# Kernel tuning notes

Measured on AMD Instinct MI355X. Metric: run time of the kernel, lower is better.

## Reference

```python
import jax, jax.numpy as jnp
import numpy as np

L, B, S, D, H, FF = 6, 32, 512, 512, 8, 2048
DK = D // H
EPS = 1e-5
GELU_C = 0.7978845608028654  # sqrt(2/pi)
INV_SQRT_DK = 1.0 / float(np.sqrt(DK))


def gelu(x):
    return 0.5 * x * (1.0 + jnp.tanh(GELU_C * (x + 0.044715 * x ** 3)))


def layernorm(x, gamma, beta):
    m = jnp.mean(x, axis=-1, keepdims=True)
    v = jnp.mean(jnp.square(x - m), axis=-1, keepdims=True)
    return gamma * (x - m) / jnp.sqrt(v + EPS) + beta


def attention(x, WQ, WK, WV, WO):
    # NOTE: the original splits columns as (d_key, n_heads) on input,
    # and merges as (n_heads * d_key) on output -- replicated faithfully.
    q = (x @ WQ).reshape(B, S, DK, H).transpose(0, 3, 1, 2)  # (B,H,S,DK)
    k = (x @ WK).reshape(B, S, DK, H).transpose(0, 3, 2, 1)  # (B,H,DK,S)
    v = (x @ WV).reshape(B, S, DK, H).transpose(0, 3, 1, 2)  # (B,H,S,DK)
    score = jax.nn.softmax(jnp.matmul(q, k) * INV_SQRT_DK, axis=-1)  # (B,H,S,S)
    o = jnp.matmul(score, v).transpose(0, 2, 1, 3).reshape(B, S, H * DK)
    return o @ WO


def setup_inputs() -> dict:
    key = jax.random.key(0)
    ks = jax.random.split(key, 8)
    sc = 0.02
    return {
        "x": jax.random.normal(ks[0], (B, S, D), jnp.float32),
        "WQ": jax.random.normal(ks[1], (L, D, D), jnp.float32) * sc,
        "WK": jax.random.normal(ks[2], (L, D, D), jnp.float32) * sc,
        "WV": jax.random.normal(ks[3], (L, D, D), jnp.float32) * sc,
        "WO": jax.random.normal(ks[4], (L, D, D), jnp.float32) * sc,
        "K1": jax.random.normal(ks[5], (L, D, FF), jnp.float32) * sc,
        "B1": jnp.zeros((L, FF), jnp.float32),
        "K2": jax.random.normal(ks[6], (L, FF, D), jnp.float32) * sc,
        "B2": jnp.zeros((L, D), jnp.float32),
        "G1": jnp.ones((L, D), jnp.float32),
        "BE1": jnp.zeros((L, D), jnp.float32),
        "G2": jnp.ones((L, D), jnp.float32),
        "BE2": jnp.zeros((L, D), jnp.float32),
    }


def reference(x, WQ, WK, WV, WO, K1, B1, K2, B2, G1, BE1, G2, BE2):
    def step(h, p):
        wq, wk, wv, wo, k1, b1, k2, b2, g1, be1, g2, be2 = p
        h = layernorm(h + attention(h, wq, wk, wv, wo), g1, be1)
        f = gelu(h @ k1 + b1) @ k2 + b2
        h = layernorm(h + f, g2, be2)
        return h, None

    out, _ = jax.lax.scan(step, x, (WQ, WK, WV, WO, K1, B1, K2, B2, G1, BE1, G2, BE2))
    return out
```

## Files before the change

kernel.cpp:

```cpp
#include <hip/hip_runtime.h>
#include <hip/hip_bf16.h>
#include <stdint.h>

#define LB 6
#define BB 32
#define SS 512
#define DD 512
#define HH 8
#define FF_ 2048
#define MM (BB*SS)

typedef unsigned short u16;
typedef __attribute__((ext_vector_type(8))) short bf16x8;
typedef __attribute__((ext_vector_type(4))) float f32x4;

#define MFMA16(a,b,c) __builtin_amdgcn_mfma_f32_16x16x32_bf16((a),(b),(c),0,0,0)
#define GLD16(g, l) __builtin_amdgcn_global_load_lds( \
    (const __attribute__((address_space(1))) unsigned int*)(g), \
    (__attribute__((address_space(3))) unsigned int*)(l), 16, 0, 0)
#define BAR() asm volatile("s_barrier" ::: "memory")
#define VMW(n) asm volatile("s_waitcnt vmcnt(" #n ")" ::: "memory")

__device__ __forceinline__ u16 f2b(float f){
  unsigned int u = __float_as_uint(f);
  u = u + 0x7FFFu + ((u >> 16) & 1u);
  return (u16)(u >> 16);
}

__device__ __forceinline__ float gelu_f(float x){
  float u2 = 1.5957691216057308f * (x + 0.044715f * x * x * x);
  return x / (1.0f + __expf(-u2));
}

__global__ __launch_bounds__(256) void k_prep(const float* __restrict__ x,
                                              float* __restrict__ h,
                                              u16* __restrict__ hb){
  int i = blockIdx.x * 256 + threadIdx.x;
  float4 v = ((const float4*)x)[i];
  ((float4*)h)[i] = v;
  uint2 p;
  p.x = (unsigned)f2b(v.x) | ((unsigned)f2b(v.y) << 16);
  p.y = (unsigned)f2b(v.z) | ((unsigned)f2b(v.w) << 16);
  ((uint2*)hb)[i] = p;
}

__global__ __launch_bounds__(256) void k_wt(const float* __restrict__ in,
                                            u16* __restrict__ out, int K, int N){
  size_t ms = (size_t)K * N;
  in  += ms * blockIdx.z;
  out += ms * blockIdx.z;
  int n0 = blockIdx.x * 64, k0 = blockIdx.y * 64;
  __shared__ float tile[64][65];
  int t = threadIdx.x;
  int c = t & 63, rb = t >> 6;
  #pragma unroll
  for (int p = 0; p < 16; p++){
    int k = p * 4 + rb;
    tile[k][c] = in[(size_t)(k0 + k) * N + (n0 + c)];
  }
  __syncthreads();
  #pragma unroll
  for (int p = 0; p < 16; p++){
    int n = p * 4 + rb;
    out[(size_t)(n0 + n) * K + (k0 + c)] = f2b(tile[c][n]);
  }
}

template<int BN, int EPI, bool PERM>
__global__ __launch_bounds__(512, 1) void k_gemm8(
    const u16* __restrict__ A,
    const u16* __restrict__ Bq, const u16* __restrict__ Bk, const u16* __restrict__ Bv,
    const float* __restrict__ bias, float* __restrict__ outF, u16* __restrict__ outH,
    int N, int K)
{
  constexpr int WM = (BN==256) ? 2 : 4;
  constexpr int MR = 16/WM;
  constexpr int MQ = MR/4;
  constexpr int BHALF = (BN==256) ? 8192 : 4096;
  constexpr int BBUF  = 2*BHALF;
  constexpr int BL    = (BN==256) ? 2 : 1;
  constexpr int HC    = (BN==256) ? 128 : 64;
  __shared__ u16 sM[32768 + 2*BBUF];

  const int t = threadIdx.x;
  const int lane = t & 63, w = t >> 6, lr = lane & 15, lh = lane >> 4;
  const int wm = (BN==256) ? (w>>2) : (w>>1);
  const int wn = (BN==256) ? (w&3)  : (w&1);
  const int bm = blockIdx.x * 256, bn = blockIdx.y * BN;
  const int NTT = K >> 6, NIT = NTT >> 1;
  const int tz = PERM ? (bn >> 9) : 0;

  const int skA = (((t>>6)&1)<<5) + (((t>>4)&3)<<3);
  const int srA = ((t>>7)<<4) + (t&15);
  const u16* gA0 = A + (size_t)(bm +       srA) * K + skA;
  const u16* gA1 = A + (size_t)(bm + 128 + srA) * K + skA;
  const u16* gBp[2][2];
  {
    const u16* Bsel = PERM ? (tz==0 ? Bq : tz==1 ? Bk : Bv) : Bq;
    #pragma unroll
    for (int h = 0; h < 2; h++){
      #pragma unroll
      for (int s = 0; s < BL; s++){
        int n = (PERM ? (bn & 511) : bn) + h*HC + srA + s*64;
        int srow = PERM ? (((n & 63) << 3) | (n >> 6)) : n;
        gBp[h][s] = Bsel + (size_t)srow * K + skA;
      }
    }
  }

  auto stageA = [&](int kt, int h){
    u16* dst = sM + (kt&1)*16384 + h*8192 + t*8;
    const u16* src = (h ? gA1 : gA0) + kt*64;
    GLD16(src, dst);
    GLD16(src + (size_t)64*K, dst + 4096);
  };
  auto stageB = [&](int kt, int h){
    u16* dst = sM + 32768 + (kt&1)*BBUF + h*BHALF + t*8;
    GLD16(gBp[h][0] + kt*64, dst);
    if constexpr (BL == 2) GLD16(gBp[h][1] + kt*64, dst + 4096);
  };

  const int ha    = (BN==256) ? wm : (wm>>1);
  const int mbase = (BN==256) ? 0  : ((wm&1)*4);
  const int hbi   = (BN==256) ? (wn>>1) : wn;
  const int nfb   = (BN==256) ? ((wn&1)*4) : 0;
  const int rdAbase = ha*8192 + lane*8;
  const int rdBbase = 32768 + hbi*BHALF + nfb*1024 + lane*8;

  f32x4 acc[MR][4];
  #pragma unroll
  for (int i = 0; i < MR; i++)
    #pragma unroll
    for (int j = 0; j < 4; j++) acc[i][j] = (f32x4){0.f,0.f,0.f,0.f};
  bf16x8 bfr[4][2];

#define RD_A(d, q, af) { _Pragma("unroll") for (int i=0;i<MQ;i++){ _Pragma("unroll") for (int ks=0;ks<2;ks++) \
    af[i][ks] = *(const bf16x8*)&sM[(d)*16384 + rdAbase + ((mbase + (q)*MQ + i)*2 + ks)*512]; } }
#define RD_B(d) { _Pragma("unroll") for (int j=0;j<4;j++){ _Pragma("unroll") for (int ks=0;ks<2;ks++) \
    bfr[j][ks] = *(const bf16x8*)&sM[(d)*BBUF + rdBbase + ((j)*2 + (ks))*512]; } }
#define FMA_Q(q, af) { __builtin_amdgcn_s_setprio(1); \
  _Pragma("unroll") for (int i=0;i<MQ;i++){ _Pragma("unroll") for (int j=0;j<4;j++){ _Pragma("unroll") for (int ks=0;ks<2;ks++) \
    acc[(q)*MQ+i][j] = MFMA16(af[i][ks], bfr[j][ks], acc[(q)*MQ+i][j]); } } \
  __builtin_amdgcn_s_setprio(0); }

  stageA(0,0); stageA(0,1); stageB(0,0); stageB(0,1); stageB(1,0); stageB(1,1);
  if constexpr (BL == 2) { VMW(4); } else { VMW(2); }
  BAR();

  for (int it = 0; it < NIT; ++it){
    const int t0 = it*2;
    const bool lastit = (it == NIT-1);
    bf16x8 af[MQ][2];
    RD_A(0,0,af); RD_B(0); stageA(t0+1, 0);            BAR(); FMA_Q(0, af); BAR();
    RD_A(0,1,af);          stageA(t0+1, 1);            BAR(); FMA_Q(1, af); BAR();
    RD_A(0,2,af); if (t0+2 < NTT) stageB(t0+2, 0);     BAR(); FMA_Q(2, af); BAR();
    RD_A(0,3,af); if (t0+2 < NTT) stageB(t0+2, 1);     BAR(); FMA_Q(3, af);
    if (lastit) { VMW(0); } else { if constexpr (BL == 2) { VMW(4); } else { VMW(2); } }
    BAR();
    RD_A(1,0,af); RD_B(1); if (t0+2 < NTT) stageA(t0+2, 0); BAR(); FMA_Q(0, af); BAR();
    RD_A(1,1,af);          if (t0+2 < NTT) stageA(t0+2, 1); BAR(); FMA_Q(1, af); BAR();
    RD_A(1,2,af); if (t0+3 < NTT) stageB(t0+3, 0);     BAR(); FMA_Q(2, af); BAR();
    RD_A(1,3,af); if (t0+3 < NTT) stageB(t0+3, 1);     BAR(); FMA_Q(3, af);
    if (!lastit) { if constexpr (BL == 2) { VMW(4); } else { VMW(2); } }
    BAR();
  }
#undef RD_A
#undef RD_B
#undef FMA_Q

  #pragma unroll
  for (int mf = 0; mf < MR; mf++){
    const int row = bm + wm*(256/WM) + mf*16 + lh*4;
    #pragma unroll
    for (int j = 0; j < 4; j++){
      const int col = (PERM ? (bn & 511) : bn) + wn*64 + j*16 + lr;
      float bv = (EPI >= 2) ? bias[col] : 0.f;
      #pragma unroll
      for (int r = 0; r < 4; r++){
        float v = acc[mf][j][r];
        size_t o = (size_t)(row + r) * N + col;
        if (PERM) o += (size_t)tz * ((size_t)MM * DD);
        if (EPI == 0) outH[o] = f2b(v);
        else if (EPI == 1) outF[o] = v;
        else if (EPI == 2) outH[o] = f2b(gelu_f(v + bv));
        else outF[o] = v + bv;
      }
    }
  }
}

__global__ __launch_bounds__(256) void k_attn(const u16* __restrict__ Q, const u16* __restrict__ Kp,
                                              const u16* __restrict__ V, u16* __restrict__ O){
  const int qt = blockIdx.x, hh = blockIdx.y, b = blockIdx.z;
  __shared__ u16 Qs[64*64];
  __shared__ u16 Ks[64*64];
  __shared__ u16 Vt[64*64];
  __shared__ u16 Ps[64*64];
  const int t = threadIdx.x, w = t >> 6, lane = t & 63, lr = lane & 15, lh = lane >> 4;
  const size_t base = ((size_t)b * SS) * DD + (size_t)hh * 64;

  const int srow = t >> 3;
  const int gcol = (((t & 7) ^ (srow & 7)) << 3);
  {
    const u16* g = Q + base + (size_t)(qt*64 + srow) * DD + gcol;
    GLD16(g,                   Qs + w*512);
    GLD16(g + (size_t)32*DD,   Qs + 2048 + w*512);
  }

  float mreg[4], lreg[4];
  f32x4 ofr[4];
  #pragma unroll
  for (int r = 0; r < 4; r++){ mreg[r] = -1e30f; lreg[r] = 0.f; }
  #pragma unroll
  for (int j = 0; j < 4; j++) ofr[j] = (f32x4){0.f,0.f,0.f,0.f};

  const int qswz = (lr & 7) << 3;

  for (int kt = 0; kt < 8; kt++){
    {
      const u16* g = Kp + base + (size_t)(kt*64 + srow) * DD + gcol;
      GLD16(g,                 Ks + w*512);
      GLD16(g + (size_t)32*DD, Ks + 2048 + w*512);
    }
    {
      const int dk0 = (t & 7) * 8, kv = (t >> 3) * 2;
      const u16* g = V + base + (size_t)(kt*64 + kv) * DD + dk0;
      uint4 r0 = *(const uint4*)g;
      uint4 r1 = *(const uint4*)(g + DD);
      const u16* e0 = (const u16*)&r0;
      const u16* e1 = (const u16*)&r1;
      #pragma unroll
      for (int i = 0; i < 8; i++){
        int dk = dk0 + i;
        int sw = ((((dk >> 3) ^ dk) & 7) << 3);
        *(unsigned int*)&Vt[dk*64 + (kv ^ sw)] =
            (unsigned int)e0[i] | ((unsigned int)e1[i] << 16);
      }
    }
    __syncthreads();

    bf16x8 a0 = *(const bf16x8*)&Qs[(w*16+lr)*64 + ((lh*8) ^ qswz)];
    bf16x8 a1 = *(const bf16x8*)&Qs[(w*16+lr)*64 + ((32 + lh*8) ^ qswz)];
    f32x4 sc[4];
    #pragma unroll
    for (int j = 0; j < 4; j++){
      bf16x8 b0 = *(const bf16x8*)&Ks[(j*16+lr)*64 + ((lh*8) ^ qswz)];
      bf16x8 b1 = *(const bf16x8*)&Ks[(j*16+lr)*64 + ((32 + lh*8) ^ qswz)];
      f32x4 z = (f32x4){0.f,0.f,0.f,0.f};
      z = MFMA16(a0, b0, z);
      z = MFMA16(a1, b1, z);
      sc[j] = z;
    }

    float pr[4][4];
    float esc[4];
    #pragma unroll
    for (int r = 0; r < 4; r++){
      float mx = fmaxf(fmaxf(sc[0][r], sc[1][r]), fmaxf(sc[2][r], sc[3][r]));
      mx = fmaxf(mx, __shfl_xor(mx, 1));
      mx = fmaxf(mx, __shfl_xor(mx, 2));
      mx = fmaxf(mx, __shfl_xor(mx, 4));
      mx = fmaxf(mx, __shfl_xor(mx, 8));
      mx *= 0.125f;
      float m2 = fmaxf(mreg[r], mx);
      float scl = __expf(mreg[r] - m2);
      mreg[r] = m2;
      float s = 0.f;
      #pragma unroll
      for (int j = 0; j < 4; j++){
        float p = __expf(sc[j][r]*0.125f - m2);
        pr[j][r] = p;
        s += p;
      }
      s += __shfl_xor(s, 1);
      s += __shfl_xor(s, 2);
      s += __shfl_xor(s, 4);
      s += __shfl_xor(s, 8);
      lreg[r] = lreg[r]*scl + s;
      esc[r] = scl;
    }

    #pragma unroll
    for (int j = 0; j < 4; j++)
      #pragma unroll
      for (int r = 0; r < 4; r++){
        int prow = w*16 + lh*4 + r;
        int pcol = j*16 + lr;
        Ps[prow*64 + (pcol ^ (((lh*4 + r) & 7) << 3))] = f2b(pr[j][r]);
      }

    #pragma unroll
    for (int j = 0; j < 4; j++)
      #pragma unroll
      for (int r = 0; r < 4; r++) ofr[j][r] *= esc[r];

    bf16x8 pa0 = *(const bf16x8*)&Ps[(w*16+lr)*64 + ((lh*8) ^ qswz)];
    bf16x8 pa1 = *(const bf16x8*)&Ps[(w*16+lr)*64 + ((32 + lh*8) ^ qswz)];
    #pragma unroll
    for (int j = 0; j < 4; j++){
      int dkr = j*16 + lr;
      int sw = ((((dkr >> 3) ^ dkr) & 7) << 3);
      bf16x8 v0 = *(const bf16x8*)&Vt[dkr*64 + ((lh*8) ^ sw)];
      bf16x8 v1 = *(const bf16x8*)&Vt[dkr*64 + ((32 + lh*8) ^ sw)];
      ofr[j] = MFMA16(pa0, v0, ofr[j]);
      ofr[j] = MFMA16(pa1, v1, ofr[j]);
    }
    __syncthreads();
  }

  #pragma unroll
  for (int j = 0; j < 4; j++)
    #pragma unroll
    for (int r = 0; r < 4; r++){
      float v = ofr[j][r] / lreg[r];
      O[base + (size_t)(qt*64 + w*16 + lh*4 + r) * DD + j*16 + lr] = f2b(v);
    }
}

__global__ __launch_bounds__(256) void k_ln(const float* __restrict__ hin, const float* __restrict__ add,
    const float* __restrict__ g, const float* __restrict__ be,
    float* __restrict__ hout, u16* __restrict__ hb){
  const int w = threadIdx.x >> 6, lane = threadIdx.x & 63;
  const size_t row = (size_t)blockIdx.x * 4 + w;
  const size_t base = row * DD + lane * 8;
  float4 xa = *(const float4*)&hin[base];
  float4 xb = *(const float4*)&hin[base + 4];
  float4 aa = *(const float4*)&add[base];
  float4 ab = *(const float4*)&add[base + 4];
  float v[8] = { xa.x+aa.x, xa.y+aa.y, xa.z+aa.z, xa.w+aa.w,
                 xb.x+ab.x, xb.y+ab.y, xb.z+ab.z, xb.w+ab.w };
  float s = 0.f, q = 0.f;
  #pragma unroll
  for (int e = 0; e < 8; e++){ s += v[e]; q += v[e]*v[e]; }
  #pragma unroll
  for (int m = 32; m >= 1; m >>= 1){ s += __shfl_xor(s, m); q += __shfl_xor(q, m); }
  float mean = s * (1.f/512.f);
  float var  = q * (1.f/512.f) - mean*mean;
  float rstd = rsqrtf(var + 1e-5f);
  float4 g0 = *(const float4*)&g[lane*8],  g1 = *(const float4*)&g[lane*8+4];
  float4 b0 = *(const float4*)&be[lane*8], b1 = *(const float4*)&be[lane*8+4];
  float gv[8] = {g0.x,g0.y,g0.z,g0.w,g1.x,g1.y,g1.z,g1.w};
  float bv[8] = {b0.x,b0.y,b0.z,b0.w,b1.x,b1.y,b1.z,b1.w};
  float o[8];
  #pragma unroll
  for (int e = 0; e < 8; e++) o[e] = gv[e] * ((v[e]-mean)*rstd) + bv[e];
  *(float4*)&hout[base]     = make_float4(o[0],o[1],o[2],o[3]);
  *(float4*)&hout[base + 4] = make_float4(o[4],o[5],o[6],o[7]);
  uint4 pk;
  pk.x = (unsigned)f2b(o[0]) | ((unsigned)f2b(o[1])<<16);
  pk.y = (unsigned)f2b(o[2]) | ((unsigned)f2b(o[3])<<16);
  pk.z = (unsigned)f2b(o[4]) | ((unsigned)f2b(o[5])<<16);
  pk.w = (unsigned)f2b(o[6]) | ((unsigned)f2b(o[7])<<16);
  *(uint4*)&hb[base] = pk;
}

extern "C" void kernel_launch(void* const* d_in, const int* in_sizes, int n_in,
                              void* d_out, int out_size, void* d_ws, size_t ws_size,
                              hipStream_t stream){
  const float* x   = (const float*)d_in[0];
  const float* WQ  = (const float*)d_in[1];
  const float* WK  = (const float*)d_in[2];
  const float* WV  = (const float*)d_in[3];
  const float* WO  = (const float*)d_in[4];
  const float* K1  = (const float*)d_in[5];
  const float* B1  = (const float*)d_in[6];
  const float* K2  = (const float*)d_in[7];
  const float* B2  = (const float*)d_in[8];
  const float* G1  = (const float*)d_in[9];
  const float* BE1 = (const float*)d_in[10];
  const float* G2  = (const float*)d_in[11];
  const float* BE2 = (const float*)d_in[12];
  float* hF = (float*)d_out;

  char* wp = (char*)d_ws;
  size_t off = 0;
  auto a16 = [&](size_t elems)->u16*{ u16* p = (u16*)(wp + off); off += elems*sizeof(u16); return p; };
  u16* WQt = a16((size_t)LB*DD*DD);
  u16* WKt = a16((size_t)LB*DD*DD);
  u16* WVt = a16((size_t)LB*DD*DD);
  u16* WOt = a16((size_t)LB*DD*DD);
  u16* K1t = a16((size_t)LB*DD*FF_);
  u16* K2t = a16((size_t)LB*DD*FF_);
  u16* hbf = a16((size_t)MM*DD);
  u16* qbf = a16((size_t)MM*DD);
  u16* kbf = a16((size_t)MM*DD);
  u16* vbf = a16((size_t)MM*DD);
  u16* abf = a16((size_t)MM*DD);
  u16* ff1 = qbf;
  float* tmpF = (float*)(wp + off); off += (size_t)MM*DD*sizeof(float);
  (void)ws_size; (void)in_sizes; (void)n_in; (void)out_size;

  k_prep<<<MM*DD/4/256, 256, 0, stream>>>(x, hF, hbf);
  k_wt<<<dim3(8,8,LB),        256, 0, stream>>>(WQ, WQt, DD, DD);
  k_wt<<<dim3(8,8,LB),        256, 0, stream>>>(WK, WKt, DD, DD);
  k_wt<<<dim3(8,8,LB),        256, 0, stream>>>(WV, WVt, DD, DD);
  k_wt<<<dim3(8,8,LB),        256, 0, stream>>>(WO, WOt, DD, DD);
  k_wt<<<dim3(FF_/64,8,LB),   256, 0, stream>>>(K1, K1t, DD, FF_);
  k_wt<<<dim3(8,FF_/64,LB),   256, 0, stream>>>(K2, K2t, FF_, DD);

  for (int l = 0; l < LB; l++){
    const u16* wq = WQt + (size_t)l*DD*DD;
    const u16* wk = WKt + (size_t)l*DD*DD;
    const u16* wv = WVt + (size_t)l*DD*DD;
    const u16* wo = WOt + (size_t)l*DD*DD;
    const u16* k1 = K1t + (size_t)l*DD*FF_;
    const u16* k2 = K2t + (size_t)l*DD*FF_;

    k_gemm8<256,0,true ><<<dim3(64,6), 512, 0, stream>>>(hbf, wq, wk, wv, nullptr, nullptr, qbf, DD, DD);
    k_attn<<<dim3(SS/64, HH, BB), 256, 0, stream>>>(qbf, kbf, vbf, abf);
    k_gemm8<128,1,false><<<dim3(64,4), 512, 0, stream>>>(abf, wo, wo, wo, nullptr, tmpF, nullptr, DD, DD);
    k_ln<<<MM/4, 256, 0, stream>>>(hF, tmpF, G1 + l*DD, BE1 + l*DD, hF, hbf);
    k_gemm8<256,2,false><<<dim3(64,8), 512, 0, stream>>>(hbf, k1, k1, k1, B1 + (size_t)l*FF_, nullptr, ff1, FF_, DD);
    k_gemm8<128,3,false><<<dim3(64,4), 512, 0, stream>>>(ff1, k2, k2, k2, B2 + l*DD, tmpF, nullptr, DD, FF_);
    k_ln<<<MM/4, 256, 0, stream>>>(hF, tmpF, G2 + l*DD, BE2 + l*DD, hF, hbf);
  }
}
```

Measured before the change: 1.854 ms.

## Double-buffer K/V in attention, enlarge query tile, retile QKV GEMM

The attention kernel now processes 128 query rows per 512-thread block and double-buffers K and V tiles in shared memory. Half the waves prefetch V into registers and the other half issue async K loads for the next tile while the current tile is computed, which drops one barrier per iteration. The grid is flattened so that heads of the same batch and query tile are adjacent, and the QKV projection GEMM switches to a 128-wide tile with twice as many blocks. This trades more shared memory and fewer blocks per CU for more overlap of memory and compute.

```diff
diff --git a/kernel.cpp b/kernel.cpp
--- a/kernel.cpp
+++ b/kernel.cpp
@@ -189,22 +189,35 @@
   }
 }
 
-__global__ __launch_bounds__(256) void k_attn(const u16* __restrict__ Q, const u16* __restrict__ Kp,
+__global__ __launch_bounds__(512) void k_attn(const u16* __restrict__ Q, const u16* __restrict__ Kp,
                                               const u16* __restrict__ V, u16* __restrict__ O){
-  const int qt = blockIdx.x, hh = blockIdx.y, b = blockIdx.z;
-  __shared__ u16 Qs[64*64];
-  __shared__ u16 Ks[64*64];
-  __shared__ u16 Vt[64*64];
-  __shared__ u16 Ps[64*64];
+  const int L = blockIdx.x;
+  const int hh = L & 7, qt = (L >> 3) & 3, b = L >> 5;
+  __shared__ u16 Qs[8192];
+  __shared__ u16 Ks[2][4096];
+  __shared__ u16 Vt[2][4096];
+  __shared__ u16 Ps[8192];
   const int t = threadIdx.x, w = t >> 6, lane = t & 63, lr = lane & 15, lh = lane >> 4;
   const size_t base = ((size_t)b * SS) * DD + (size_t)hh * 64;
 
-  const int srow = t >> 3;
-  const int gcol = (((t & 7) ^ (srow & 7)) << 3);
   {
-    const u16* g = Q + base + (size_t)(qt*64 + srow) * DD + gcol;
-    GLD16(g,                   Qs + w*512);
-    GLD16(g + (size_t)32*DD,   Qs + 2048 + w*512);
+    const int srow = t >> 3;
+    const int gcol = (((t & 7) ^ (srow & 7)) << 3);
+    const u16* g = Q + base + (size_t)(qt*128 + srow) * DD + gcol;
+    GLD16(g,                 Qs + w*512);
+    GLD16(g + (size_t)64*DD, Qs + 4096 + w*512);
+  }
+  const int vdk0 = (t & 7) * 8, vkv = ((t >> 3) & 31) * 2;
+  const int srow2 = ((w & 3) * 8) + (lane >> 3);
+  const int gcol2 = (((lane & 7) ^ (srow2 & 7)) << 3);
+  uint4 rv0, rv1;
+  if (w < 4){
+    const u16* g = V + base + (size_t)vkv * DD + vdk0;
+    rv0 = *(const uint4*)g; rv1 = *(const uint4*)(g + DD);
+  } else {
+    const u16* g = Kp + base + (size_t)srow2 * DD + gcol2;
+    GLD16(g,                 Ks[0] + (w-4)*512);
+    GLD16(g + (size_t)32*DD, Ks[0] + 2048 + (w-4)*512);
   }
 
   float mreg[4], lreg[4];
@@ -217,35 +230,38 @@
   const int qswz = (lr & 7) << 3;
 
   for (int kt = 0; kt < 8; kt++){
-    {
-      const u16* g = Kp + base + (size_t)(kt*64 + srow) * DD + gcol;
-      GLD16(g,                 Ks + w*512);
-      GLD16(g + (size_t)32*DD, Ks + 2048 + w*512);
-    }
-    {
-      const int dk0 = (t & 7) * 8, kv = (t >> 3) * 2;
-      const u16* g = V + base + (size_t)(kt*64 + kv) * DD + dk0;
-      uint4 r0 = *(const uint4*)g;
-      uint4 r1 = *(const uint4*)(g + DD);
-      const u16* e0 = (const u16*)&r0;
-      const u16* e1 = (const u16*)&r1;
+    const int bix = kt & 1;
+    if (w < 4){
+      const u16* e0 = (const u16*)&rv0;
+      const u16* e1 = (const u16*)&rv1;
       #pragma unroll
       for (int i = 0; i < 8; i++){
-        int dk = dk0 + i;
+        int dk = vdk0 + i;
         int sw = ((((dk >> 3) ^ dk) & 7) << 3);
-        *(unsigned int*)&Vt[dk*64 + (kv ^ sw)] =
+        *(unsigned int*)&Vt[bix][dk*64 + (vkv ^ sw)] =
             (unsigned int)e0[i] | ((unsigned int)e1[i] << 16);
       }
     }
     __syncthreads();
+
+    if (kt < 7){
+      if (w < 4){
+        const u16* g = V + base + (size_t)((kt+1)*64 + vkv) * DD + vdk0;
+        rv0 = *(const uint4*)g; rv1 = *(const uint4*)(g + DD);
+      } else {
+        const u16* g = Kp + base + (size_t)((kt+1)*64 + srow2) * DD + gcol2;
+        GLD16(g,                 Ks[bix^1] + (w-4)*512);
+        GLD16(g + (size_t)32*DD, Ks[bix^1] + 2048 + (w-4)*512);
+      }
+    }
 
     bf16x8 a0 = *(const bf16x8*)&Qs[(w*16+lr)*64 + ((lh*8) ^ qswz)];
     bf16x8 a1 = *(const bf16x8*)&Qs[(w*16+lr)*64 + ((32 + lh*8) ^ qswz)];
     f32x4 sc[4];
     #pragma unroll
     for (int j = 0; j < 4; j++){
-      bf16x8 b0 = *(const bf16x8*)&Ks[(j*16+lr)*64 + ((lh*8) ^ qswz)];
-      bf16x8 b1 = *(const bf16x8*)&Ks[(j*16+lr)*64 + ((32 + lh*8) ^ qswz)];
+      bf16x8 b0 = *(const bf16x8*)&Ks[bix][(j*16+lr)*64 + ((lh*8) ^ qswz)];
+      bf16x8 b1 = *(const bf16x8*)&Ks[bix][(j*16+lr)*64 + ((32 + lh*8) ^ qswz)];
       f32x4 z = (f32x4){0.f,0.f,0.f,0.f};
       z = MFMA16(a0, b0, z);
       z = MFMA16(a1, b1, z);
@@ -300,12 +316,11 @@
     for (int j = 0; j < 4; j++){
       int dkr = j*16 + lr;
       int sw = ((((dkr >> 3) ^ dkr) & 7) << 3);
-      bf16x8 v0 = *(const bf16x8*)&Vt[dkr*64 + ((lh*8) ^ sw)];
-      bf16x8 v1 = *(const bf16x8*)&Vt[dkr*64 + ((32 + lh*8) ^ sw)];
+      bf16x8 v0 = *(const bf16x8*)&Vt[bix][dkr*64 + ((lh*8) ^ sw)];
+      bf16x8 v1 = *(const bf16x8*)&Vt[bix][dkr*64 + ((32 + lh*8) ^ sw)];
       ofr[j] = MFMA16(pa0, v0, ofr[j]);
       ofr[j] = MFMA16(pa1, v1, ofr[j]);
     }
-    __syncthreads();
   }
 
   #pragma unroll
@@ -313,7 +328,7 @@
     #pragma unroll
     for (int r = 0; r < 4; r++){
       float v = ofr[j][r] / lreg[r];
-      O[base + (size_t)(qt*64 + w*16 + lh*4 + r) * DD + j*16 + lr] = f2b(v);
+      O[base + (size_t)(qt*128 + w*16 + lh*4 + r) * DD + j*16 + lr] = f2b(v);
     }
 }
 
@@ -406,8 +421,8 @@
     const u16* k1 = K1t + (size_t)l*DD*FF_;
     const u16* k2 = K2t + (size_t)l*DD*FF_;
 
-    k_gemm8<256,0,true ><<<dim3(64,6), 512, 0, stream>>>(hbf, wq, wk, wv, nullptr, nullptr, qbf, DD, DD);
-    k_attn<<<dim3(SS/64, HH, BB), 256, 0, stream>>>(qbf, kbf, vbf, abf);
+    k_gemm8<128,0,true ><<<dim3(64,12), 512, 0, stream>>>(hbf, wq, wk, wv, nullptr, nullptr, qbf, DD, DD);
+    k_attn<<<dim3(1024), 512, 0, stream>>>(qbf, kbf, vbf, abf);
     k_gemm8<128,1,false><<<dim3(64,4), 512, 0, stream>>>(abf, wo, wo, wo, nullptr, tmpF, nullptr, DD, DD);
     k_ln<<<MM/4, 256, 0, stream>>>(hF, tmpF, G1 + l*DD, BE1 + l*DD, hF, hbf);
     k_gemm8<256,2,false><<<dim3(64,8), 512, 0, stream>>>(hbf, k1, k1, k1, B1 + (size_t)l*FF_, nullptr, ff1, FF_, DD);
```

After: 1.828 ms. About the same (-1.4%).
